# Kernel optimization log

Measured on AMD Instinct MI355X. Metric: run time of the kernel, lower is better.

Reference implementation:

```python
import jax, jax.numpy as jnp
import numpy as np

TEMPERATURE = 1.0  # spec.temperature, clamped to >=1e-6 in the original
NEG_INF = -1000000000.0


def setup_inputs() -> dict:
    key = jax.random.key(0)
    k_x, k_w1, k_b1, k_w2, k_b2 = jax.random.split(key, 5)
    N, d_in, d_h, E = 32768, 1024, 256, 64
    s1 = 1.0 / np.sqrt(d_in)
    s2 = 1.0 / np.sqrt(d_h)
    return {
        "stage_input": jax.random.normal(k_x, (N, d_in), dtype=jnp.float32),
        "w1": jax.random.uniform(k_w1, (d_in, d_h), jnp.float32, -s1, s1),
        "b1": jax.random.uniform(k_b1, (d_h,), jnp.float32, -s1, s1),
        "w2": jax.random.uniform(k_w2, (d_h, E), jnp.float32, -s2, s2),
        "b2": jax.random.uniform(k_b2, (E,), jnp.float32, -s2, s2),
        "top_k": 8,
    }


def reference(stage_input, w1, b1, w2, b2, top_k):
    # Router MLP: Linear -> ReLU -> (Dropout, eval=identity) -> Linear
    h = jax.nn.relu(stage_input @ w1 + b1)          # [N, d_hidden]
    logits = h @ w2 + b2                             # [N, E]

    scaled = logits / TEMPERATURE
    E = scaled.shape[-1]
    k = min(int(top_k), E)
    if 0 < k < E:
        vals, idx = jax.lax.top_k(scaled, k)         # [N, k]
        rows = jnp.arange(scaled.shape[0])[:, None]
        masked = jnp.full_like(scaled, NEG_INF).at[rows, idx].set(vals)
    else:
        masked = scaled

    probs = jax.nn.softmax(masked, axis=-1)          # [N, E]
    return logits, masked, probs
```

## Files before the change

### kernel.cpp

```cpp
#include <hip/hip_runtime.h>
#include <hip/hip_bf16.h>
#include <float.h>


#define N_ROWS 32768
#define D_IN   1024
#define D_H    256
#define N_E    64
#define NEG_INF_VAL (-1000000000.0f)

typedef _Float16 f16x8 __attribute__((ext_vector_type(8)));
typedef float    f32x4  __attribute__((ext_vector_type(4)));
typedef float    f32x16 __attribute__((ext_vector_type(16)));

#define MM32(A, B, C) __builtin_amdgcn_mfma_f32_32x32x16_f16(A, B, C, 0, 0, 0)
#define MM16(A, B, C) __builtin_amdgcn_mfma_f32_16x16x32_f16(A, B, C, 0, 0, 0)

#define KBAR()                                         \
  do {                                                 \
    asm volatile("s_waitcnt lgkmcnt(0)" ::: "memory"); \
    __builtin_amdgcn_s_barrier();                      \
    asm volatile("" ::: "memory");                     \
  } while (0)

__global__ __launch_bounds__(256) void split_weights_kernel(
    const float* __restrict__ w1, const float* __restrict__ w2,
    _Float16* __restrict__ w1pk_h, _Float16* __restrict__ w1pk_l,
    _Float16* __restrict__ w2pk_h, _Float16* __restrict__ w2pk_l) {
  int idx = blockIdx.x * 256 + threadIdx.x;
  if (idx < D_IN * D_H) {
    const int k = idx >> 8;
    const int n = idx & 255;
    const float v = w1[idx];
    const _Float16 hi = (_Float16)v;
    const _Float16 lo = (_Float16)(v - (float)hi);
    const int wv = n >> 6, nf = (n >> 5) & 1, l31 = n & 31;
    const int it = k >> 6, kf = (k >> 4) & 3, kg = (k >> 3) & 1, j = k & 7;
    const int lane = kg * 32 + l31;
    const int off = ((((wv * 16 + it) * 4 + kf) * 2 + nf) * 64 + lane) * 8 + j;
    w1pk_h[off] = hi;
    w1pk_l[off] = lo;
  } else {
    idx -= D_IN * D_H;
    const int k = idx >> 6;
    const int e = idx & 63;
    const float v = w2[idx];
    const _Float16 hi = (_Float16)v;
    const _Float16 lo = (_Float16)(v - (float)hi);
    const int s = k >> 5, kg = (k >> 3) & 3, j = k & 7;
    const int f = e >> 4, cc = e & 15;
    const int lane = kg * 16 + cc;
    const int off = ((s * 4 + f) * 64 + lane) * 8 + j;
    w2pk_h[off] = hi;
    w2pk_l[off] = lo;
  }
}

__global__ __launch_bounds__(256, 2) void fused_router_kernel(
    const float* __restrict__ x, const _Float16* __restrict__ w1pk_h,
    const _Float16* __restrict__ w1pk_l, const float* __restrict__ b1,
    const _Float16* __restrict__ w2pk_h, const _Float16* __restrict__ w2pk_l,
    const float* __restrict__ b2, const int* __restrict__ topk_p,
    float* __restrict__ out_logits, float* __restrict__ out_masked,
    float* __restrict__ out_probs) {
  __shared__ char lds[65536];

  const int t  = threadIdx.x;
  const int m0 = blockIdx.x * 64;

  const int srow = t >> 2;
  const int skb2 = (t & 3) * 32;
  const int sw   = (srow & 7) << 4;

  const int wv   = t >> 6;
  const int lane = t & 63;
  const int l31  = lane & 31;
  const int kg   = lane >> 5;

  const float* xrowp = x + (size_t)(m0 + srow) * D_IN + (t & 3) * 16;
  const f16x8* bph = (const f16x8*)w1pk_h;
  const f16x8* bpl = (const f16x8*)w1pk_l;

  f32x16 acc00, acc01, acc10, acc11;
#pragma unroll
  for (int i = 0; i < 16; ++i) {
    acc00[i] = 0.f; acc01[i] = 0.f; acc10[i] = 0.f; acc11[i] = 0.f;
  }

  f16x8 uh00, uh01, uh10, uh11, uh20, uh21, uh30, uh31;
  f16x8 ul00, ul01, ul10, ul11, ul20, ul21, ul30, ul31;
  f16x8 vh00, vh01, vh10, vh11, vh20, vh21, vh30, vh31;
  f16x8 vl00, vl01, vl10, vl11, vl20, vl21, vl30, vl31;

#define STAGE_WRITE(bufi, q0, q1, q2, q3)                                    \
  do {                                                                       \
    const float vv[16] = {q0.x, q0.y, q0.z, q0.w, q1.x, q1.y, q1.z, q1.w,    \
                          q2.x, q2.y, q2.z, q2.w, q3.x, q3.y, q3.z, q3.w};   \
    f16x8 hi0, hi1, lo0, lo1;                                                \
    _Pragma("unroll") for (int j = 0; j < 8; ++j) {                          \
      const _Float16 hv = (_Float16)vv[j];                                   \
      hi0[j] = hv; lo0[j] = (_Float16)(vv[j] - (float)hv);                   \
    }                                                                        \
    _Pragma("unroll") for (int j = 0; j < 8; ++j) {                          \
      const _Float16 hv = (_Float16)vv[8 + j];                               \
      hi1[j] = hv; lo1[j] = (_Float16)(vv[8 + j] - (float)hv);               \
    }                                                                        \
    char* bb = lds + (bufi) * 16384 + srow * 256;                            \
    *(f16x8*)(bb + ((skb2 + 0) ^ sw)) = hi0;                                 \
    *(f16x8*)(bb + ((skb2 + 16) ^ sw)) = hi1;                                \
    *(f16x8*)(bb + 128 + ((skb2 + 0) ^ sw)) = lo0;                           \
    *(f16x8*)(bb + 128 + ((skb2 + 16) ^ sw)) = lo1;                          \
  } while (0)

#define LOAD_B(BH, BL, itv)                                                  \
  do {                                                                       \
    const int ch = (wv * 16 + (itv)) * 512 + lane;                           \
    BH##00 = bph[ch + 0 * 64]; BH##01 = bph[ch + 1 * 64];                    \
    BH##10 = bph[ch + 2 * 64]; BH##11 = bph[ch + 3 * 64];                    \
    BH##20 = bph[ch + 4 * 64]; BH##21 = bph[ch + 5 * 64];                    \
    BH##30 = bph[ch + 6 * 64]; BH##31 = bph[ch + 7 * 64];                    \
    BL##00 = bpl[ch + 0 * 64]; BL##01 = bpl[ch + 1 * 64];                    \
    BL##10 = bpl[ch + 2 * 64]; BL##11 = bpl[ch + 3 * 64];                    \
    BL##20 = bpl[ch + 4 * 64]; BL##21 = bpl[ch + 5 * 64];                    \
    BL##30 = bpl[ch + 6 * 64]; BL##31 = bpl[ch + 7 * 64];                    \
  } while (0)

#define MFMA_KF(rb, kfv, BH0, BL0, BH1, BL1)                                 \
  do {                                                                       \
    const int kb = (kfv) * 32 + kg * 16;                                     \
    const char* ap0 = (rb) + l31 * 256 + (kb ^ ((l31 & 7) << 4));            \
    const char* ap1 = ap0 + 32 * 256;                                        \
    const f16x8 ah0 = *(const f16x8*)(ap0);                                  \
    const f16x8 al0 = *(const f16x8*)(ap0 + 128);                            \
    const f16x8 ah1 = *(const f16x8*)(ap1);                                  \
    const f16x8 al1 = *(const f16x8*)(ap1 + 128);                            \
    acc00 = MM32(al0, BH0, acc00); acc01 = MM32(al0, BH1, acc01);            \
    acc10 = MM32(al1, BH0, acc10); acc11 = MM32(al1, BH1, acc11);            \
    acc00 = MM32(ah0, BL0, acc00); acc01 = MM32(ah0, BL1, acc01);            \
    acc10 = MM32(ah1, BL0, acc10); acc11 = MM32(ah1, BL1, acc11);            \
    acc00 = MM32(ah0, BH0, acc00); acc01 = MM32(ah0, BH1, acc01);            \
    acc10 = MM32(ah1, BH0, acc10); acc11 = MM32(ah1, BH1, acc11);            \
  } while (0)

#define GSTEP(ITV, LB, CH, CL, NH, NL)                                       \
  do {                                                                       \
    float4 p0, p1, p2, p3;                                                   \
    const bool more = (ITV) + 1 < 16;                                        \
    if (more) {                                                              \
      const float4* xp = (const float4*)(xrowp + ((ITV) + 1) * 64);          \
      p0 = xp[0]; p1 = xp[1]; p2 = xp[2]; p3 = xp[3];                        \
      LOAD_B(NH, NL, (ITV) + 1);                                             \
    }                                                                        \
    const char* rb = lds + (LB) * 16384;                                     \
    MFMA_KF(rb, 0, CH##00, CL##00, CH##01, CL##01);                          \
    MFMA_KF(rb, 1, CH##10, CL##10, CH##11, CL##11);                          \
    MFMA_KF(rb, 2, CH##20, CL##20, CH##21, CL##21);                          \
    MFMA_KF(rb, 3, CH##30, CL##30, CH##31, CL##31);                          \
    if (more) STAGE_WRITE(1 - (LB), p0, p1, p2, p3);                         \
    KBAR();                                                                  \
  } while (0)

  {
    const float4* xp = (const float4*)(xrowp);
    const float4 q0 = xp[0], q1 = xp[1], q2 = xp[2], q3 = xp[3];
    STAGE_WRITE(0, q0, q1, q2, q3);
    LOAD_B(uh, ul, 0);
  }
  KBAR();

#pragma unroll
  for (int ii = 0; ii < 8; ++ii) {
    GSTEP(2 * ii,     0, uh, ul, vh, vl);
    GSTEP(2 * ii + 1, 1, vh, vl, uh, ul);
  }

#define EPI(ACC, MF, NF)                                                     \
  do {                                                                       \
    const int colg = wv * 64 + (NF) * 32 + l31;                              \
    const float bias = b1[colg];                                             \
    _Pragma("unroll") for (int r = 0; r < 16; ++r) {                         \
      const int row = (MF) * 32 + (r & 3) + 8 * (r >> 2) + 4 * kg;           \
      const float hv = fmaxf(ACC[r] + bias, 0.0f);                           \
      const _Float16 hhi = (_Float16)hv;                                     \
      const _Float16 hlo = (_Float16)(hv - (float)hhi);                      \
      const int byo = row * 512 + ((colg * 2) ^ ((row & 7) << 4));           \
      *(_Float16*)(lds + byo) = hhi;                                         \
      *(_Float16*)(lds + 32768 + byo) = hlo;                                 \
    }                                                                        \
  } while (0)

  EPI(acc00, 0, 0); EPI(acc01, 0, 1); EPI(acc10, 1, 0); EPI(acc11, 1, 1);
#undef EPI
  KBAR();

  const int c   = lane & 15;
  const int kg4 = lane >> 4;
  const int rowl = wv * 16 + c;
  const int sw2 = (rowl & 7) << 4;
  const char* hhb = lds + rowl * 512;
  const char* hlb = lds + 32768 + rowl * 512;
  const f16x8* b2ph = (const f16x8*)w2pk_h;
  const f16x8* b2pl = (const f16x8*)w2pk_l;

  f32x4 r0 = {0.f, 0.f, 0.f, 0.f};
  f32x4 r1 = {0.f, 0.f, 0.f, 0.f};
  f32x4 r2 = {0.f, 0.f, 0.f, 0.f};
  f32x4 r3 = {0.f, 0.f, 0.f, 0.f};

#pragma unroll
  for (int s = 0; s < 8; ++s) {
    const int kb = (s * 64 + kg4 * 16) ^ sw2;
    const f16x8 ah = *(const f16x8*)(hhb + kb);
    const f16x8 al = *(const f16x8*)(hlb + kb);
    const int ch = s * 256 + lane;
    const f16x8 bh0 = b2ph[ch +   0], bh1 = b2ph[ch +  64];
    const f16x8 bh2 = b2ph[ch + 128], bh3 = b2ph[ch + 192];
    const f16x8 bl0 = b2pl[ch +   0], bl1 = b2pl[ch +  64];
    const f16x8 bl2 = b2pl[ch + 128], bl3 = b2pl[ch + 192];
    r0 = MM16(al, bh0, r0); r1 = MM16(al, bh1, r1);
    r2 = MM16(al, bh2, r2); r3 = MM16(al, bh3, r3);
    r0 = MM16(ah, bl0, r0); r1 = MM16(ah, bl1, r1);
    r2 = MM16(ah, bl2, r2); r3 = MM16(ah, bl3, r3);
    r0 = MM16(ah, bh0, r0); r1 = MM16(ah, bh1, r1);
    r2 = MM16(ah, bh2, r2); r3 = MM16(ah, bh3, r3);
  }

  const int K = topk_p[0];
  const bool doMask = (K > 0 && K < N_E);
  const float b2v0 = b2[c], b2v1 = b2[16 + c], b2v2 = b2[32 + c],
              b2v3 = b2[48 + c];
  const int rowbase = m0 + wv * 16;

#pragma unroll
  for (int r = 0; r < 4; ++r) {
    const int row = rowbase + kg4 * 4 + r;
    float* lg = out_logits + (size_t)row * N_E;
    float* mk = out_masked + (size_t)row * N_E;
    float* pb = out_probs  + (size_t)row * N_E;

    const float v0 = r0[r] + b2v0;
    const float v1 = r1[r] + b2v1;
    const float v2 = r2[r] + b2v2;
    const float v3 = r3[r] + b2v3;
    lg[c] = v0; lg[16 + c] = v1; lg[32 + c] = v2; lg[48 + c] = v3;

    bool s0 = true, s1 = true, s2 = true, s3 = true;
    if (doMask) {
      s0 = s1 = s2 = s3 = false;
      float c0 = v0, c1 = v1, c2 = v2, c3 = v3;
      for (int it = 0; it < K; ++it) {
        float m = c0; int mi = c;
        if (c1 > m) { m = c1; mi = 16 + c; }
        if (c2 > m) { m = c2; mi = 32 + c; }
        if (c3 > m) { m = c3; mi = 48 + c; }
#pragma unroll
        for (int off = 1; off <= 8; off <<= 1) {
          const float om = __shfl_xor(m, off);
          const int   oi = __shfl_xor(mi, off);
          if (om > m || (om == m && oi < mi)) { m = om; mi = oi; }
        }
        if ((mi & 15) == c) {
          const int f = mi >> 4;
          s0 = s0 || (f == 0); c0 = (f == 0) ? -FLT_MAX : c0;
          s1 = s1 || (f == 1); c1 = (f == 1) ? -FLT_MAX : c1;
          s2 = s2 || (f == 2); c2 = (f == 2) ? -FLT_MAX : c2;
          s3 = s3 || (f == 3); c3 = (f == 3) ? -FLT_MAX : c3;
        }
      }
    }
    const float m0v = s0 ? v0 : NEG_INF_VAL;
    const float m1v = s1 ? v1 : NEG_INF_VAL;
    const float m2v = s2 ? v2 : NEG_INF_VAL;
    const float m3v = s3 ? v3 : NEG_INF_VAL;
    mk[c] = m0v; mk[16 + c] = m1v; mk[32 + c] = m2v; mk[48 + c] = m3v;

    float mx = fmaxf(fmaxf(m0v, m1v), fmaxf(m2v, m3v));
#pragma unroll
    for (int off = 1; off <= 8; off <<= 1) mx = fmaxf(mx, __shfl_xor(mx, off));
    const float e0 = __expf(m0v - mx);
    const float e1 = __expf(m1v - mx);
    const float e2 = __expf(m2v - mx);
    const float e3 = __expf(m3v - mx);
    float sm = e0 + e1 + e2 + e3;
#pragma unroll
    for (int off = 1; off <= 8; off <<= 1) sm += __shfl_xor(sm, off);
    const float inv = 1.0f / sm;
    pb[c] = e0 * inv; pb[16 + c] = e1 * inv; pb[32 + c] = e2 * inv;
    pb[48 + c] = e3 * inv;
  }
#undef GSTEP
#undef MFMA_KF
#undef LOAD_B
#undef STAGE_WRITE
}

extern "C" void kernel_launch(void* const* d_in, const int* in_sizes, int n_in,
                              void* d_out, int out_size, void* d_ws,
                              size_t ws_size, hipStream_t stream) {
  const float* x  = (const float*)d_in[0];
  const float* w1 = (const float*)d_in[1];
  const float* b1 = (const float*)d_in[2];
  const float* w2 = (const float*)d_in[3];
  const float* b2 = (const float*)d_in[4];
  const int* topk = (const int*)d_in[5];

  char* ws = (char*)d_ws;
  _Float16* w1pk_h = (_Float16*)(ws);
  _Float16* w1pk_l = (_Float16*)(ws + 524288);
  _Float16* w2pk_h = (_Float16*)(ws + 1048576);
  _Float16* w2pk_l = (_Float16*)(ws + 1081344);

  float* out_logits = (float*)d_out;
  float* out_masked = out_logits + (size_t)N_ROWS * N_E;
  float* out_probs  = out_masked + (size_t)N_ROWS * N_E;

  split_weights_kernel<<<(D_IN * D_H + D_H * N_E) / 256, 256, 0, stream>>>(
      w1, w2, w1pk_h, w1pk_l, w2pk_h, w2pk_l);

  fused_router_kernel<<<N_ROWS / 64, 256, 0, stream>>>(
      x, w1pk_h, w1pk_l, b1, w2pk_h, w2pk_l, b2, topk, out_logits, out_masked,
      out_probs);
}
```

Baseline: 84.55 us.

## Double threads per block to 512, each wave owning 32 hidden columns

Raises the fused router block from 4 to 8 waves. Each wave now computes a 64x32 tile of the first GEMM instead of 64x64, which halves per-thread accumulator and B-fragment registers, and the W1 packing layout changes to match. X staging is spread over twice as many threads. The second GEMM and the top-k/softmax epilogue stay on the first 4 waves while the other 4 sit idle. The aim is more latency hiding per CU, at the cost of idle waves in the epilogue and possible occupancy limits from 64KB of LDS per block.

```diff
diff --git a/kernel.cpp b/kernel.cpp
--- a/kernel.cpp
+++ b/kernel.cpp
@@ -34,10 +34,10 @@
     const float v = w1[idx];
     const _Float16 hi = (_Float16)v;
     const _Float16 lo = (_Float16)(v - (float)hi);
-    const int wv = n >> 6, nf = (n >> 5) & 1, l31 = n & 31;
+    const int wv8 = n >> 5, l31 = n & 31;
     const int it = k >> 6, kf = (k >> 4) & 3, kg = (k >> 3) & 1, j = k & 7;
     const int lane = kg * 32 + l31;
-    const int off = ((((wv * 16 + it) * 4 + kf) * 2 + nf) * 64 + lane) * 8 + j;
+    const int off = (((wv8 * 16 + it) * 4 + kf) * 64 + lane) * 8 + j;
     w1pk_h[off] = hi;
     w1pk_l[off] = lo;
   } else {
@@ -56,7 +56,7 @@
   }
 }
 
-__global__ __launch_bounds__(256, 2) void fused_router_kernel(
+__global__ __launch_bounds__(512, 2) void fused_router_kernel(
     const float* __restrict__ x, const _Float16* __restrict__ w1pk_h,
     const _Float16* __restrict__ w1pk_l, const float* __restrict__ b1,
     const _Float16* __restrict__ w2pk_h, const _Float16* __restrict__ w2pk_l,
@@ -68,8 +68,8 @@
   const int t  = threadIdx.x;
   const int m0 = blockIdx.x * 64;
 
-  const int srow = t >> 2;
-  const int skb2 = (t & 3) * 32;
+  const int srow = t >> 3;
+  const int slot = (t & 7) * 16;
   const int sw   = (srow & 7) << 4;
 
   const int wv   = t >> 6;
@@ -77,55 +77,40 @@
   const int l31  = lane & 31;
   const int kg   = lane >> 5;
 
-  const float* xrowp = x + (size_t)(m0 + srow) * D_IN + (t & 3) * 16;
+  const float* xrowp = x + (size_t)(m0 + srow) * D_IN + (t & 7) * 8;
   const f16x8* bph = (const f16x8*)w1pk_h;
   const f16x8* bpl = (const f16x8*)w1pk_l;
 
-  f32x16 acc00, acc01, acc10, acc11;
-#pragma unroll
-  for (int i = 0; i < 16; ++i) {
-    acc00[i] = 0.f; acc01[i] = 0.f; acc10[i] = 0.f; acc11[i] = 0.f;
-  }
-
-  f16x8 uh00, uh01, uh10, uh11, uh20, uh21, uh30, uh31;
-  f16x8 ul00, ul01, ul10, ul11, ul20, ul21, ul30, ul31;
-  f16x8 vh00, vh01, vh10, vh11, vh20, vh21, vh30, vh31;
-  f16x8 vl00, vl01, vl10, vl11, vl20, vl21, vl30, vl31;
-
-#define STAGE_WRITE(bufi, q0, q1, q2, q3)                                    \
-  do {                                                                       \
-    const float vv[16] = {q0.x, q0.y, q0.z, q0.w, q1.x, q1.y, q1.z, q1.w,    \
-                          q2.x, q2.y, q2.z, q2.w, q3.x, q3.y, q3.z, q3.w};   \
-    f16x8 hi0, hi1, lo0, lo1;                                                \
+  f32x16 acc0, acc1;
+#pragma unroll
+  for (int i = 0; i < 16; ++i) { acc0[i] = 0.f; acc1[i] = 0.f; }
+
+  f16x8 uh0, uh1, uh2, uh3, ul0, ul1, ul2, ul3;
+  f16x8 vh0, vh1, vh2, vh3, vl0, vl1, vl2, vl3;
+
+#define STAGE_WRITE(bufi, q0, q1)                                            \
+  do {                                                                       \
+    const float vv[8] = {q0.x, q0.y, q0.z, q0.w, q1.x, q1.y, q1.z, q1.w};    \
+    f16x8 hi8, lo8;                                                          \
     _Pragma("unroll") for (int j = 0; j < 8; ++j) {                          \
       const _Float16 hv = (_Float16)vv[j];                                   \
-      hi0[j] = hv; lo0[j] = (_Float16)(vv[j] - (float)hv);                   \
-    }                                                                        \
-    _Pragma("unroll") for (int j = 0; j < 8; ++j) {                          \
-      const _Float16 hv = (_Float16)vv[8 + j];                               \
-      hi1[j] = hv; lo1[j] = (_Float16)(vv[8 + j] - (float)hv);               \
+      hi8[j] = hv; lo8[j] = (_Float16)(vv[j] - (float)hv);                   \
     }                                                                        \
     char* bb = lds + (bufi) * 16384 + srow * 256;                            \
-    *(f16x8*)(bb + ((skb2 + 0) ^ sw)) = hi0;                                 \
-    *(f16x8*)(bb + ((skb2 + 16) ^ sw)) = hi1;                                \
-    *(f16x8*)(bb + 128 + ((skb2 + 0) ^ sw)) = lo0;                           \
-    *(f16x8*)(bb + 128 + ((skb2 + 16) ^ sw)) = lo1;                          \
-  } while (0)
-
-#define LOAD_B(BH, BL, itv)                                                  \
-  do {                                                                       \
-    const int ch = (wv * 16 + (itv)) * 512 + lane;                           \
-    BH##00 = bph[ch + 0 * 64]; BH##01 = bph[ch + 1 * 64];                    \
-    BH##10 = bph[ch + 2 * 64]; BH##11 = bph[ch + 3 * 64];                    \
-    BH##20 = bph[ch + 4 * 64]; BH##21 = bph[ch + 5 * 64];                    \
-    BH##30 = bph[ch + 6 * 64]; BH##31 = bph[ch + 7 * 64];                    \
-    BL##00 = bpl[ch + 0 * 64]; BL##01 = bpl[ch + 1 * 64];                    \
-    BL##10 = bpl[ch + 2 * 64]; BL##11 = bpl[ch + 3 * 64];                    \
-    BL##20 = bpl[ch + 4 * 64]; BL##21 = bpl[ch + 5 * 64];                    \
-    BL##30 = bpl[ch + 6 * 64]; BL##31 = bpl[ch + 7 * 64];                    \
-  } while (0)
-
-#define MFMA_KF(rb, kfv, BH0, BL0, BH1, BL1)                                 \
+    *(f16x8*)(bb + (slot ^ sw)) = hi8;                                       \
+    *(f16x8*)(bb + 128 + (slot ^ sw)) = lo8;                                 \
+  } while (0)
+
+#define LOAD_B(BH0, BH1, BH2, BH3, BL0, BL1, BL2, BL3, itv)                  \
+  do {                                                                       \
+    const int ch = (wv * 16 + (itv)) * 256 + lane;                           \
+    BH0 = bph[ch + 0 * 64]; BH1 = bph[ch + 1 * 64];                          \
+    BH2 = bph[ch + 2 * 64]; BH3 = bph[ch + 3 * 64];                          \
+    BL0 = bpl[ch + 0 * 64]; BL1 = bpl[ch + 1 * 64];                          \
+    BL2 = bpl[ch + 2 * 64]; BL3 = bpl[ch + 3 * 64];                          \
+  } while (0)
+
+#define MFMA_KF(rb, kfv, BH, BL)                                             \
   do {                                                                       \
     const int kb = (kfv) * 32 + kg * 16;                                     \
     const char* ap0 = (rb) + l31 * 256 + (kb ^ ((l31 & 7) << 4));            \
@@ -134,49 +119,49 @@
     const f16x8 al0 = *(const f16x8*)(ap0 + 128);                            \
     const f16x8 ah1 = *(const f16x8*)(ap1);                                  \
     const f16x8 al1 = *(const f16x8*)(ap1 + 128);                            \
-    acc00 = MM32(al0, BH0, acc00); acc01 = MM32(al0, BH1, acc01);            \
-    acc10 = MM32(al1, BH0, acc10); acc11 = MM32(al1, BH1, acc11);            \
-    acc00 = MM32(ah0, BL0, acc00); acc01 = MM32(ah0, BL1, acc01);            \
-    acc10 = MM32(ah1, BL0, acc10); acc11 = MM32(ah1, BL1, acc11);            \
-    acc00 = MM32(ah0, BH0, acc00); acc01 = MM32(ah0, BH1, acc01);            \
-    acc10 = MM32(ah1, BH0, acc10); acc11 = MM32(ah1, BH1, acc11);            \
-  } while (0)
-
-#define GSTEP(ITV, LB, CH, CL, NH, NL)                                       \
-  do {                                                                       \
-    float4 p0, p1, p2, p3;                                                   \
+    acc0 = MM32(al0, BH, acc0); acc1 = MM32(al1, BH, acc1);                  \
+    acc0 = MM32(ah0, BL, acc0); acc1 = MM32(ah1, BL, acc1);                  \
+    acc0 = MM32(ah0, BH, acc0); acc1 = MM32(ah1, BH, acc1);                  \
+  } while (0)
+
+#define GSTEP(ITV, LB, CH0, CH1, CH2, CH3, CL0, CL1, CL2, CL3,               \
+              NH0, NH1, NH2, NH3, NL0, NL1, NL2, NL3)                        \
+  do {                                                                       \
+    float4 p0, p1;                                                           \
     const bool more = (ITV) + 1 < 16;                                        \
     if (more) {                                                              \
       const float4* xp = (const float4*)(xrowp + ((ITV) + 1) * 64);          \
-      p0 = xp[0]; p1 = xp[1]; p2 = xp[2]; p3 = xp[3];                        \
-      LOAD_B(NH, NL, (ITV) + 1);                                             \
+      p0 = xp[0]; p1 = xp[1];                                                \
+      LOAD_B(NH0, NH1, NH2, NH3, NL0, NL1, NL2, NL3, (ITV) + 1);             \
     }                                                                        \
     const char* rb = lds + (LB) * 16384;                                     \
-    MFMA_KF(rb, 0, CH##00, CL##00, CH##01, CL##01);                          \
-    MFMA_KF(rb, 1, CH##10, CL##10, CH##11, CL##11);                          \
-    MFMA_KF(rb, 2, CH##20, CL##20, CH##21, CL##21);                          \
-    MFMA_KF(rb, 3, CH##30, CL##30, CH##31, CL##31);                          \
-    if (more) STAGE_WRITE(1 - (LB), p0, p1, p2, p3);                         \
+    MFMA_KF(rb, 0, CH0, CL0);                                                \
+    MFMA_KF(rb, 1, CH1, CL1);                                                \
+    MFMA_KF(rb, 2, CH2, CL2);                                                \
+    MFMA_KF(rb, 3, CH3, CL3);                                                \
+    if (more) STAGE_WRITE(1 - (LB), p0, p1);                                 \
     KBAR();                                                                  \
   } while (0)
 
   {
     const float4* xp = (const float4*)(xrowp);
-    const float4 q0 = xp[0], q1 = xp[1], q2 = xp[2], q3 = xp[3];
-    STAGE_WRITE(0, q0, q1, q2, q3);
-    LOAD_B(uh, ul, 0);
+    const float4 q0 = xp[0], q1 = xp[1];
+    STAGE_WRITE(0, q0, q1);
+    LOAD_B(uh0, uh1, uh2, uh3, ul0, ul1, ul2, ul3, 0);
   }
   KBAR();
 
 #pragma unroll
   for (int ii = 0; ii < 8; ++ii) {
-    GSTEP(2 * ii,     0, uh, ul, vh, vl);
-    GSTEP(2 * ii + 1, 1, vh, vl, uh, ul);
+    GSTEP(2 * ii, 0, uh0, uh1, uh2, uh3, ul0, ul1, ul2, ul3,
+          vh0, vh1, vh2, vh3, vl0, vl1, vl2, vl3);
+    GSTEP(2 * ii + 1, 1, vh0, vh1, vh2, vh3, vl0, vl1, vl2, vl3,
+          uh0, uh1, uh2, uh3, ul0, ul1, ul2, ul3);
   }
 
-#define EPI(ACC, MF, NF)                                                     \
-  do {                                                                       \
-    const int colg = wv * 64 + (NF) * 32 + l31;                              \
+#define EPI(ACC, MF)                                                         \
+  do {                                                                       \
+    const int colg = wv * 32 + l31;                                          \
     const float bias = b1[colg];                                             \
     _Pragma("unroll") for (int r = 0; r < 16; ++r) {                         \
       const int row = (MF) * 32 + (r & 3) + 8 * (r >> 2) + 4 * kg;           \
@@ -189,104 +174,107 @@
     }                                                                        \
   } while (0)
 
-  EPI(acc00, 0, 0); EPI(acc01, 0, 1); EPI(acc10, 1, 0); EPI(acc11, 1, 1);
+  EPI(acc0, 0); EPI(acc1, 1);
 #undef EPI
   KBAR();
 
-  const int c   = lane & 15;
-  const int kg4 = lane >> 4;
-  const int rowl = wv * 16 + c;
-  const int sw2 = (rowl & 7) << 4;
-  const char* hhb = lds + rowl * 512;
-  const char* hlb = lds + 32768 + rowl * 512;
-  const f16x8* b2ph = (const f16x8*)w2pk_h;
-  const f16x8* b2pl = (const f16x8*)w2pk_l;
-
-  f32x4 r0 = {0.f, 0.f, 0.f, 0.f};
-  f32x4 r1 = {0.f, 0.f, 0.f, 0.f};
-  f32x4 r2 = {0.f, 0.f, 0.f, 0.f};
-  f32x4 r3 = {0.f, 0.f, 0.f, 0.f};
-
-#pragma unroll
-  for (int s = 0; s < 8; ++s) {
-    const int kb = (s * 64 + kg4 * 16) ^ sw2;
-    const f16x8 ah = *(const f16x8*)(hhb + kb);
-    const f16x8 al = *(const f16x8*)(hlb + kb);
-    const int ch = s * 256 + lane;
-    const f16x8 bh0 = b2ph[ch +   0], bh1 = b2ph[ch +  64];
-    const f16x8 bh2 = b2ph[ch + 128], bh3 = b2ph[ch + 192];
-    const f16x8 bl0 = b2pl[ch +   0], bl1 = b2pl[ch +  64];
-    const f16x8 bl2 = b2pl[ch + 128], bl3 = b2pl[ch + 192];
-    r0 = MM16(al, bh0, r0); r1 = MM16(al, bh1, r1);
-    r2 = MM16(al, bh2, r2); r3 = MM16(al, bh3, r3);
-    r0 = MM16(ah, bl0, r0); r1 = MM16(ah, bl1, r1);
-    r2 = MM16(ah, bl2, r2); r3 = MM16(ah, bl3, r3);
-    r0 = MM16(ah, bh0, r0); r1 = MM16(ah, bh1, r1);
-    r2 = MM16(ah, bh2, r2); r3 = MM16(ah, bh3, r3);
-  }
-
-  const int K = topk_p[0];
-  const bool doMask = (K > 0 && K < N_E);
-  const float b2v0 = b2[c], b2v1 = b2[16 + c], b2v2 = b2[32 + c],
-              b2v3 = b2[48 + c];
-  const int rowbase = m0 + wv * 16;
-
-#pragma unroll
-  for (int r = 0; r < 4; ++r) {
-    const int row = rowbase + kg4 * 4 + r;
-    float* lg = out_logits + (size_t)row * N_E;
-    float* mk = out_masked + (size_t)row * N_E;
-    float* pb = out_probs  + (size_t)row * N_E;
-
-    const float v0 = r0[r] + b2v0;
-    const float v1 = r1[r] + b2v1;
-    const float v2 = r2[r] + b2v2;
-    const float v3 = r3[r] + b2v3;
-    lg[c] = v0; lg[16 + c] = v1; lg[32 + c] = v2; lg[48 + c] = v3;
-
-    bool s0 = true, s1 = true, s2 = true, s3 = true;
-    if (doMask) {
-      s0 = s1 = s2 = s3 = false;
-      float c0 = v0, c1 = v1, c2 = v2, c3 = v3;
-      for (int it = 0; it < K; ++it) {
-        float m = c0; int mi = c;
-        if (c1 > m) { m = c1; mi = 16 + c; }
-        if (c2 > m) { m = c2; mi = 32 + c; }
-        if (c3 > m) { m = c3; mi = 48 + c; }
-#pragma unroll
-        for (int off = 1; off <= 8; off <<= 1) {
-          const float om = __shfl_xor(m, off);
-          const int   oi = __shfl_xor(mi, off);
-          if (om > m || (om == m && oi < mi)) { m = om; mi = oi; }
-        }
-        if ((mi & 15) == c) {
-          const int f = mi >> 4;
-          s0 = s0 || (f == 0); c0 = (f == 0) ? -FLT_MAX : c0;
-          s1 = s1 || (f == 1); c1 = (f == 1) ? -FLT_MAX : c1;
-          s2 = s2 || (f == 2); c2 = (f == 2) ? -FLT_MAX : c2;
-          s3 = s3 || (f == 3); c3 = (f == 3) ? -FLT_MAX : c3;
+  if (wv < 4) {
+    const int c   = lane & 15;
+    const int kg4 = lane >> 4;
+    const int rowl = wv * 16 + c;
+    const int sw2 = (rowl & 7) << 4;
+    const char* hhb = lds + rowl * 512;
+    const char* hlb = lds + 32768 + rowl * 512;
+    const f16x8* b2ph = (const f16x8*)w2pk_h;
+    const f16x8* b2pl = (const f16x8*)w2pk_l;
+
+    f32x4 r0 = {0.f, 0.f, 0.f, 0.f};
+    f32x4 r1 = {0.f, 0.f, 0.f, 0.f};
+    f32x4 r2 = {0.f, 0.f, 0.f, 0.f};
+    f32x4 r3 = {0.f, 0.f, 0.f, 0.f};
+
+#pragma unroll
+    for (int s = 0; s < 8; ++s) {
+      const int kb = (s * 64 + kg4 * 16) ^ sw2;
+      const f16x8 ah = *(const f16x8*)(hhb + kb);
+      const f16x8 al = *(const f16x8*)(hlb + kb);
+      const int ch = s * 256 + lane;
+      const f16x8 bh0 = b2ph[ch +   0], bh1 = b2ph[ch +  64];
+      const f16x8 bh2 = b2ph[ch + 128], bh3 = b2ph[ch + 192];
+      const f16x8 bl0 = b2pl[ch +   0], bl1 = b2pl[ch +  64];
+      const f16x8 bl2 = b2pl[ch + 128], bl3 = b2pl[ch + 192];
+      r0 = MM16(al, bh0, r0); r1 = MM16(al, bh1, r1);
+      r2 = MM16(al, bh2, r2); r3 = MM16(al, bh3, r3);
+      r0 = MM16(ah, bl0, r0); r1 = MM16(ah, bl1, r1);
+      r2 = MM16(ah, bl2, r2); r3 = MM16(ah, bl3, r3);
+      r0 = MM16(ah, bh0, r0); r1 = MM16(ah, bh1, r1);
+      r2 = MM16(ah, bh2, r2); r3 = MM16(ah, bh3, r3);
+    }
+
+    const int K = topk_p[0];
+    const bool doMask = (K > 0 && K < N_E);
+    const float b2v0 = b2[c], b2v1 = b2[16 + c], b2v2 = b2[32 + c],
+                b2v3 = b2[48 + c];
+    const int rowbase = m0 + wv * 16;
+
+#pragma unroll
+    for (int r = 0; r < 4; ++r) {
+      const int row = rowbase + kg4 * 4 + r;
+      float* lg = out_logits + (size_t)row * N_E;
+      float* mk = out_masked + (size_t)row * N_E;
+      float* pb = out_probs  + (size_t)row * N_E;
+
+      const float v0 = r0[r] + b2v0;
+      const float v1 = r1[r] + b2v1;
+      const float v2 = r2[r] + b2v2;
+      const float v3 = r3[r] + b2v3;
+      lg[c] = v0; lg[16 + c] = v1; lg[32 + c] = v2; lg[48 + c] = v3;
+
+      bool s0 = true, s1 = true, s2 = true, s3 = true;
+      if (doMask) {
+        s0 = s1 = s2 = s3 = false;
+        float c0 = v0, c1 = v1, c2 = v2, c3 = v3;
+        for (int it = 0; it < K; ++it) {
+          float m = c0; int mi = c;
+          if (c1 > m) { m = c1; mi = 16 + c; }
+          if (c2 > m) { m = c2; mi = 32 + c; }
+          if (c3 > m) { m = c3; mi = 48 + c; }
+#pragma unroll
+          for (int off = 1; off <= 8; off <<= 1) {
+            const float om = __shfl_xor(m, off);
+            const int   oi = __shfl_xor(mi, off);
+            if (om > m || (om == m && oi < mi)) { m = om; mi = oi; }
+          }
+          if ((mi & 15) == c) {
+            const int f = mi >> 4;
+            s0 = s0 || (f == 0); c0 = (f == 0) ? -FLT_MAX : c0;
+            s1 = s1 || (f == 1); c1 = (f == 1) ? -FLT_MAX : c1;
+            s2 = s2 || (f == 2); c2 = (f == 2) ? -FLT_MAX : c2;
+            s3 = s3 || (f == 3); c3 = (f == 3) ? -FLT_MAX : c3;
+          }
         }
       }
+      const float m0v = s0 ? v0 : NEG_INF_VAL;
+      const float m1v = s1 ? v1 : NEG_INF_VAL;
+      const float m2v = s2 ? v2 : NEG_INF_VAL;
+      const float m3v = s3 ? v3 : NEG_INF_VAL;
+      mk[c] = m0v; mk[16 + c] = m1v; mk[32 + c] = m2v; mk[48 + c] = m3v;
+
+      float mx = fmaxf(fmaxf(m0v, m1v), fmaxf(m2v, m3v));
+#pragma unroll
+      for (int off = 1; off <= 8; off <<= 1)
+        mx = fmaxf(mx, __shfl_xor(mx, off));
+      const float e0 = __expf(m0v - mx);
+      const float e1 = __expf(m1v - mx);
+      const float e2 = __expf(m2v - mx);
+      const float e3 = __expf(m3v - mx);
+      float sm = e0 + e1 + e2 + e3;
+#pragma unroll
+      for (int off = 1; off <= 8; off <<= 1) sm += __shfl_xor(sm, off);
+      const float inv = 1.0f / sm;
+      pb[c] = e0 * inv; pb[16 + c] = e1 * inv; pb[32 + c] = e2 * inv;
+      pb[48 + c] = e3 * inv;
     }
-    const float m0v = s0 ? v0 : NEG_INF_VAL;
-    const float m1v = s1 ? v1 : NEG_INF_VAL;
-    const float m2v = s2 ? v2 : NEG_INF_VAL;
-    const float m3v = s3 ? v3 : NEG_INF_VAL;
-    mk[c] = m0v; mk[16 + c] = m1v; mk[32 + c] = m2v; mk[48 + c] = m3v;
-
-    float mx = fmaxf(fmaxf(m0v, m1v), fmaxf(m2v, m3v));
-#pragma unroll
-    for (int off = 1; off <= 8; off <<= 1) mx = fmaxf(mx, __shfl_xor(mx, off));
-    const float e0 = __expf(m0v - mx);
-    const float e1 = __expf(m1v - mx);
-    const float e2 = __expf(m2v - mx);
-    const float e3 = __expf(m3v - mx);
-    float sm = e0 + e1 + e2 + e3;
-#pragma unroll
-    for (int off = 1; off <= 8; off <<= 1) sm += __shfl_xor(sm, off);
-    const float inv = 1.0f / sm;
-    pb[c] = e0 * inv; pb[16 + c] = e1 * inv; pb[32 + c] = e2 * inv;
-    pb[48 + c] = e3 * inv;
   }
 #undef GSTEP
 #undef MFMA_KF
@@ -317,7 +305,7 @@
   split_weights_kernel<<<(D_IN * D_H + D_H * N_E) / 256, 256, 0, stream>>>(
       w1, w2, w1pk_h, w1pk_l, w2pk_h, w2pk_l);
 
-  fused_router_kernel<<<N_ROWS / 64, 256, 0, stream>>>(
+  fused_router_kernel<<<N_ROWS / 64, 512, 0, stream>>>(
       x, w1pk_h, w1pk_l, b1, w2pk_h, w2pk_l, b2, topk, out_logits, out_masked,
       out_probs);
 }
```

After: 82.52 us. -2.4%, faster.
